# Performance work log

Hardware: AMD Instinct MI355X
Metric: run time of the kernel (lower is better)

## Reference

```python
import jax, jax.numpy as jnp
import numpy as np

B, T, D, H = 2, 4096, 768, 12
DK = D // H

def setup_inputs() -> dict:
    key = jax.random.key(0)
    ks = jax.random.split(key, 5)
    scale = 1.0 / np.sqrt(D)
    x = jax.random.normal(ks[0], (B, T, D), dtype=jnp.float32)
    WQ = jax.random.normal(ks[1], (D, D), dtype=jnp.float32) * scale
    WK = jax.random.normal(ks[2], (D, D), dtype=jnp.float32) * scale
    WV = jax.random.normal(ks[3], (D, D), dtype=jnp.float32) * scale
    Wproj = jax.random.normal(ks[4], (D, D), dtype=jnp.float32) * scale
    return {"x": x, "WQ": WQ, "WK": WK, "WV": WV, "Wproj": Wproj}

def reference(x, WQ, WK, WV, Wproj):
    # Weights stored as [in, out] (torch Linear weight transposed): y = x @ W
    def split_heads(y):
        return y.reshape(B, T, H, DK).transpose(0, 2, 1, 3)  # [B,H,T,DK]
    Q = split_heads(x @ WQ)
    K = split_heads(x @ WK)
    V = split_heads(x @ WV)
    score = jnp.einsum('bhqd,bhkd->bhqk', Q, K) * (DK ** -0.5)  # [B,H,T,T]
    attn = jax.nn.softmax(score, axis=-1)
    out = jnp.einsum('bhqk,bhkd->bhqd', attn, V)  # [B,H,T,DK]
    out = out.transpose(0, 2, 1, 3).reshape(B, T, D)
    return out @ Wproj
```

## Files before the change

### kernel.cpp

```cpp
#include <hip/hip_runtime.h>
#include <stdint.h>

#define B_ 2
#define T_ 4096
#define D_ 768
#define H_ 12
#define DK_ 64
#define BH_ 24

typedef unsigned short u16;
typedef unsigned int u32;
typedef __bf16 bf16x8 __attribute__((ext_vector_type(8)));
typedef float f32x4 __attribute__((ext_vector_type(4)));
typedef short s16x8 __attribute__((ext_vector_type(8)));

__device__ __forceinline__ float exp2_raw(float x) {
#if __has_builtin(__builtin_amdgcn_exp2f)
    return __builtin_amdgcn_exp2f(x);
#else
    float y; asm("v_exp_f32 %0, %1" : "=v"(y) : "v"(x)); return y;
#endif
}

__device__ __forceinline__ f32x4 mfma16(bf16x8 a, bf16x8 b, f32x4 c) {
    return __builtin_amdgcn_mfma_f32_16x16x32_bf16(a, b, c, 0, 0, 0);
}

__device__ __forceinline__ u16 f2bf(float f) {
    union { float f; u32 u; } v; v.f = f;
    u32 r = v.u + 0x7FFFu + ((v.u >> 16) & 1u);
    return (u16)(r >> 16);
}

__device__ __forceinline__ u32 pack2bf(float lo, float hi) {
    union { float f; u32 u; } a, b; a.f = lo; b.f = hi;
    return __builtin_amdgcn_perm(b.u + 0x8000u, a.u + 0x8000u, 0x07060302u);
}

__device__ __forceinline__ void gll16(const u16* g, u16* l) {
    __builtin_amdgcn_global_load_lds(
        (const __attribute__((address_space(1))) u32*)g,
        (__attribute__((address_space(3))) u32*)l, 16, 0, 0);
}

__global__ __launch_bounds__(256) void convert_x_kernel(
    const float* __restrict__ x, u16* __restrict__ xb)
{
    int i = (blockIdx.x * 256 + threadIdx.x) * 8;
    float4 a = *(const float4*)&x[i];
    float4 b = *(const float4*)&x[i + 4];
    uint4 dd;
    dd.x = pack2bf(a.x, a.y); dd.y = pack2bf(a.z, a.w);
    dd.z = pack2bf(b.x, b.y); dd.w = pack2bf(b.z, b.w);
    *(uint4*)&xb[i] = dd;
}

__global__ __launch_bounds__(256) void wtrans_kernel(
    const float* __restrict__ w0, const float* __restrict__ w1,
    const float* __restrict__ w2, const float* __restrict__ w3,
    u16* __restrict__ out)
{
    __shared__ u16 tile[32][33];
    const float* src = (blockIdx.z == 0) ? w0 : (blockIdx.z == 1) ? w1 : (blockIdx.z == 2) ? w2 : w3;
    u16* dst = out + (size_t)blockIdx.z * D_ * D_;
    int tx = threadIdx.x, ty = threadIdx.y;
    int x0 = blockIdx.x * 32, y0 = blockIdx.y * 32;
    for (int i = ty; i < 32; i += 8) tile[i][tx] = f2bf(src[(size_t)(y0 + i) * D_ + x0 + tx]);
    __syncthreads();
    for (int i = ty; i < 32; i += 8) dst[(size_t)(x0 + i) * D_ + y0 + tx] = tile[tx][i];
}

template<int MODE>
__global__ __launch_bounds__(256) void gemm_bt(
    const u16* __restrict__ A, const u16* __restrict__ Bt, void* __restrict__ outv)
{
    __shared__ u16 As[128 * 64];
    __shared__ u16 Bs[128 * 64];
    const int K = 768;
    int tid = threadIdx.x;
    int lane = tid & 63, wave = tid >> 6;
    int r = lane & 15, quad = lane >> 4;
    int rx = r & 7;
    int m0 = blockIdx.y * 128, n0 = blockIdx.x * 128;
    int wrow = (wave >> 1) * 64, wcol = (wave & 1) * 64;

    int srow = wave * 32 + (lane >> 3);
    int scol = ((lane & 7) ^ (lane >> 3)) * 8;
    const u16* Ag = A + (size_t)(m0 + srow) * K + scol;
    const u16* Bg = Bt + (size_t)(n0 + srow) * K + scol;

    f32x4 acc[4][4];
    #pragma unroll
    for (int i = 0; i < 4; i++)
        #pragma unroll
        for (int j = 0; j < 4; j++)
            #pragma unroll
            for (int e = 0; e < 4; e++) acc[i][j][e] = 0.f;

    for (int k0 = 0; k0 < K; k0 += 64) {
        __syncthreads();
        #pragma unroll
        for (int j = 0; j < 4; j++) {
            gll16(Ag + (size_t)j * 8 * K + k0, As + (wave * 32 + j * 8) * 64);
            gll16(Bg + (size_t)j * 8 * K + k0, Bs + (wave * 32 + j * 8) * 64);
        }
        __syncthreads();
        #pragma unroll
        for (int ks = 0; ks < 2; ks++) {
            int swz = ((ks * 4 + quad) ^ rx) * 8;
            bf16x8 af[4], bfr[4];
            #pragma unroll
            for (int mi = 0; mi < 4; mi++)
                af[mi] = *(const bf16x8*)&As[(wrow + mi * 16 + r) * 64 + swz];
            #pragma unroll
            for (int ni = 0; ni < 4; ni++)
                bfr[ni] = *(const bf16x8*)&Bs[(wcol + ni * 16 + r) * 64 + swz];
            #pragma unroll
            for (int mi = 0; mi < 4; mi++)
                #pragma unroll
                for (int ni = 0; ni < 4; ni++)
                    acc[mi][ni] = mfma16(af[mi], bfr[ni], acc[mi][ni]);
        }
    }

    if (MODE == 0) {
        u16* out = (u16*)outv;
        int which = n0 / D_;
        int nb = n0 % D_;
        const size_t HS = (size_t)B_ * H_ * T_ * DK_;
        if (which == 2) {
            u16* vt = out + 2 * HS;
            #pragma unroll
            for (int mi = 0; mi < 4; mi++) {
                int mg = m0 + wrow + mi * 16 + quad * 4;
                int b = mg >> 12, t = mg & 4095;
                #pragma unroll
                for (int ni = 0; ni < 4; ni++) {
                    int ng = nb + wcol + ni * 16 + r;
                    int h = ng >> 6, dk = ng & 63;
                    uint2 d;
                    d.x = pack2bf(acc[mi][ni][0], acc[mi][ni][1]);
                    d.y = pack2bf(acc[mi][ni][2], acc[mi][ni][3]);
                    *(uint2*)&vt[(((size_t)(b * H_ + h)) * DK_ + dk) * T_ + t] = d;
                }
            }
        } else {
            const float cf = (which == 0) ? 0.18033688011112042f : 1.0f;
            size_t wbase = (size_t)which * HS;
            #pragma unroll
            for (int mi = 0; mi < 4; mi++) {
                #pragma unroll
                for (int ni = 0; ni < 4; ni++) {
                    int ng = nb + wcol + ni * 16 + r;
                    int h = ng >> 6, dk = ng & 63;
                    #pragma unroll
                    for (int e = 0; e < 4; e++) {
                        int mg = m0 + wrow + mi * 16 + quad * 4 + e;
                        int b = mg >> 12, t = mg & 4095;
                        out[wbase + (((size_t)(b * H_ + h)) * T_ + t) * DK_ + dk]
                            = f2bf(acc[mi][ni][e] * cf);
                    }
                }
            }
        }
    } else {
        float* out = (float*)outv;
        #pragma unroll
        for (int mi = 0; mi < 4; mi++)
            #pragma unroll
            for (int ni = 0; ni < 4; ni++)
                #pragma unroll
                for (int e = 0; e < 4; e++)
                    out[(size_t)(m0 + wrow + mi * 16 + quad * 4 + e) * D_ + n0 + wcol + ni * 16 + r]
                        = acc[mi][ni][e];
    }
}

__global__ __launch_bounds__(256, 3) void attn_kernel(
    const u16* __restrict__ Q, const u16* __restrict__ K,
    const u16* __restrict__ VT, float* __restrict__ pO, float* __restrict__ pL)
{
    __shared__ u16 Ks[64 * 64];
    __shared__ u16 Vs[64 * 64];
    __shared__ u16 Pt[256 * 64];

    int tid = threadIdx.x;
    int lane = tid & 63, w = tid >> 6;
    int r = lane & 15, quad = lane >> 4;
    int rx = r & 7;
    int bh = blockIdx.y;
    int q0 = blockIdx.x * 256;
    int z = blockIdx.z;

    bf16x8 qf[4][2];
    #pragma unroll
    for (int qi = 0; qi < 4; qi++) {
        const u16* Qb = Q + ((size_t)bh * T_ + q0 + w * 64 + qi * 16 + r) * DK_;
        qf[qi][0] = *(const bf16x8*)(Qb + quad * 8);
        qf[qi][1] = *(const bf16x8*)(Qb + 32 + quad * 8);
    }

    bf16x8 ones;
    #pragma unroll
    for (int j = 0; j < 8; j++) ones[j] = (__bf16)1.0f;

    f32x4 o[4][4];
    f32x4 lacc[4];
    #pragma unroll
    for (int qi = 0; qi < 4; qi++) {
        #pragma unroll
        for (int e = 0; e < 4; e++) lacc[qi][e] = 0.f;
        #pragma unroll
        for (int n = 0; n < 4; n++)
            #pragma unroll
            for (int e = 0; e < 4; e++) o[qi][n][e] = 0.f;
    }

    u16* Pw = &Pt[w * 64 * 64];
    int kb0 = z * (T_ / 2), kb1 = kb0 + T_ / 2;

    for (int kb = kb0; kb < kb1; kb += 64) {
        __syncthreads();
        #pragma unroll
        for (int i = 0; i < 2; i++) {
            int c = tid + i * 256;
            int row = c >> 3, gc = c & 7;
            int lc = gc ^ (row & 7);
            *(bf16x8*)&Ks[row * 64 + lc * 8] =
                *(const bf16x8*)&K[((size_t)bh * T_ + kb + row) * DK_ + gc * 8];
            *(bf16x8*)&Vs[row * 64 + lc * 8] =
                *(const bf16x8*)&VT[((size_t)bh * DK_ + row) * T_ + kb + gc * 8];
        }
        __syncthreads();

        #pragma unroll
        for (int n = 0; n < 4; n++) {
            int krow = n * 16 + r;
            bf16x8 kf0 = *(const bf16x8*)&Ks[krow * 64 + ((quad ^ rx)) * 8];
            bf16x8 kf1 = *(const bf16x8*)&Ks[krow * 64 + (((4 + quad) ^ rx)) * 8];
            int c8 = 2 * n + (quad >> 1);
            #pragma unroll
            for (int qi = 0; qi < 4; qi++) {
                f32x4 zz;
                #pragma unroll
                for (int e = 0; e < 4; e++) zz[e] = 0.f;
                zz = mfma16(kf0, qf[qi][0], zz);
                zz = mfma16(kf1, qf[qi][1], zz);
                float p0 = exp2_raw(zz[0]), p1 = exp2_raw(zz[1]);
                float p2 = exp2_raw(zz[2]), p3 = exp2_raw(zz[3]);
                uint2 d;
                d.x = pack2bf(p0, p1);
                d.y = pack2bf(p2, p3);
                *(uint2*)&Pw[(qi * 16 + r) * 64 + (c8 ^ rx) * 8 + (quad & 1) * 4] = d;
            }
        }

        #pragma unroll
        for (int ks2 = 0; ks2 < 2; ks2++) {
            int swz = ((ks2 * 4 + quad) ^ rx) * 8;
            bf16x8 vf[4];
            #pragma unroll
            for (int ndk = 0; ndk < 4; ndk++)
                vf[ndk] = *(const bf16x8*)&Vs[(ndk * 16 + r) * 64 + swz];
            #pragma unroll
            for (int qi = 0; qi < 4; qi++) {
                bf16x8 pf = *(const bf16x8*)&Pw[(qi * 16 + r) * 64 + swz];
                lacc[qi] = mfma16(ones, pf, lacc[qi]);
                #pragma unroll
                for (int ndk = 0; ndk < 4; ndk++)
                    o[qi][ndk] = mfma16(vf[ndk], pf, o[qi][ndk]);
            }
        }
    }

    const size_t SP = (size_t)BH_ * T_ * DK_;
    #pragma unroll
    for (int qi = 0; qi < 4; qi++) {
        int q = q0 + w * 64 + qi * 16 + r;
        float* base = pO + (size_t)z * SP + ((size_t)bh * T_ + q) * DK_;
        #pragma unroll
        for (int ndk = 0; ndk < 4; ndk++)
            *(f32x4*)&base[ndk * 16 + quad * 4] = o[qi][ndk];
    }
    if (quad == 0) {
        #pragma unroll
        for (int qi = 0; qi < 4; qi++)
            pL[(size_t)z * BH_ * T_ + (size_t)bh * T_ + q0 + w * 64 + qi * 16 + r]
                = lacc[qi][0];
    }
}

__global__ __launch_bounds__(256) void combine_kernel(
    const float* __restrict__ pO, const float* __restrict__ pL, u16* __restrict__ AO)
{
    const size_t SP = (size_t)BH_ * T_ * DK_;
    int bh = blockIdx.y;
    int b = bh / H_, h = bh % H_;
    int q = blockIdx.x * 64 + (threadIdx.x >> 2);
    int dk0 = (threadIdx.x & 3) * 16;
    size_t idx = ((size_t)bh * T_ + q) * DK_ + dk0;
    float l0 = pL[(size_t)bh * T_ + q];
    float l1 = pL[(size_t)BH_ * T_ + (size_t)bh * T_ + q];
    float inv = 1.0f / (l0 + l1);
    u16* dst = AO + ((size_t)b * T_ + q) * D_ + h * DK_ + dk0;
    #pragma unroll
    for (int i = 0; i < 2; i++) {
        float4 a0 = *(const float4*)&pO[idx + i * 8];
        float4 a1 = *(const float4*)&pO[idx + i * 8 + 4];
        float4 b0 = *(const float4*)&pO[SP + idx + i * 8];
        float4 b1 = *(const float4*)&pO[SP + idx + i * 8 + 4];
        uint4 dd;
        dd.x = pack2bf((a0.x + b0.x) * inv, (a0.y + b0.y) * inv);
        dd.y = pack2bf((a0.z + b0.z) * inv, (a0.w + b0.w) * inv);
        dd.z = pack2bf((a1.x + b1.x) * inv, (a1.y + b1.y) * inv);
        dd.w = pack2bf((a1.z + b1.z) * inv, (a1.w + b1.w) * inv);
        *(uint4*)&dst[i * 8] = dd;
    }
}

extern "C" void kernel_launch(void* const* d_in, const int* in_sizes, int n_in,
                              void* d_out, int out_size, void* d_ws, size_t ws_size,
                              hipStream_t stream)
{
    const float* x  = (const float*)d_in[0];
    const float* wq = (const float*)d_in[1];
    const float* wk = (const float*)d_in[2];
    const float* wv = (const float*)d_in[3];
    const float* wp = (const float*)d_in[4];

    u16* ws = (u16*)d_ws;
    const size_t XS = (size_t)B_ * T_ * D_;
    const size_t WT = (size_t)D_ * D_;
    const size_t HS = (size_t)B_ * H_ * T_ * DK_;
    u16* xb = ws;
    u16* wt = xb + XS;
    u16* q  = wt + 4 * WT;
    u16* k  = q + HS;
    u16* vt = k + HS;
    u16* ao = vt + HS;
    float* pL = (float*)(ao + HS);
    float* pO = pL + 2 * (size_t)BH_ * T_;

    convert_x_kernel<<<dim3(3072), 256, 0, stream>>>(x, xb);
    wtrans_kernel<<<dim3(24, 24, 4), dim3(32, 8), 0, stream>>>(wq, wk, wv, wp, wt);
    gemm_bt<0><<<dim3(18, 64), 256, 0, stream>>>(xb, wt, q);
    attn_kernel<<<dim3(16, 24, 2), 256, 0, stream>>>(q, k, vt, pO, pL);
    combine_kernel<<<dim3(64, 24), 256, 0, stream>>>(pO, pL, ao);
    gemm_bt<1><<<dim3(6, 64), 256, 0, stream>>>(ao, wt + 3 * WT, d_out);
}
```

Before: 295.3 us.

## Split attention keys four ways, shrink P tile, store bf16 partials

The key range of the attention kernel is split four ways instead of two, doubling the number of blocks. The per-wave P staging buffer is halved by interleaving score computation and PV accumulation in two 32-key halves, and the occupancy hint rises from 3 to 5. K/V tiles are now loaded straight into LDS with global_load_lds instead of passing through registers. Partial outputs are written in bf16 and merged by a rewritten combine kernel, which cuts partial-sum traffic at the cost of some precision and extra combine reads.

Measured after the change: 1.122 ms. 3.8x slower.

```diff
diff --git a/kernel.cpp b/kernel.cpp
--- a/kernel.cpp
+++ b/kernel.cpp
@@ -7,6 +7,7 @@
 #define H_ 12
 #define DK_ 64
 #define BH_ 24
+#define ZSPLIT 4
 
 typedef unsigned short u16;
 typedef unsigned int u32;
@@ -30,6 +31,10 @@
     union { float f; u32 u; } v; v.f = f;
     u32 r = v.u + 0x7FFFu + ((v.u >> 16) & 1u);
     return (u16)(r >> 16);
+}
+
+__device__ __forceinline__ float bf2f(u16 u) {
+    union { u32 u; float f; } v; v.u = ((u32)u) << 16; return v.f;
 }
 
 __device__ __forceinline__ u32 pack2bf(float lo, float hi) {
@@ -176,18 +181,18 @@
     }
 }
 
-__global__ __launch_bounds__(256, 3) void attn_kernel(
+__global__ __launch_bounds__(256, 5) void attn_kernel(
     const u16* __restrict__ Q, const u16* __restrict__ K,
-    const u16* __restrict__ VT, float* __restrict__ pO, float* __restrict__ pL)
+    const u16* __restrict__ VT, u16* __restrict__ pOb, float* __restrict__ pL)
 {
     __shared__ u16 Ks[64 * 64];
     __shared__ u16 Vs[64 * 64];
-    __shared__ u16 Pt[256 * 64];
+    __shared__ u16 Pt[256 * 32];
 
     int tid = threadIdx.x;
     int lane = tid & 63, w = tid >> 6;
     int r = lane & 15, quad = lane >> 4;
-    int rx = r & 7;
+    int rx = r & 7, r3 = r & 3;
     int bh = blockIdx.y;
     int q0 = blockIdx.x * 256;
     int z = blockIdx.z;
@@ -216,55 +221,57 @@
             for (int e = 0; e < 4; e++) o[qi][n][e] = 0.f;
     }
 
-    u16* Pw = &Pt[w * 64 * 64];
-    int kb0 = z * (T_ / 2), kb1 = kb0 + T_ / 2;
-
-    for (int kb = kb0; kb < kb1; kb += 64) {
+    u16* Pw = &Pt[w * 64 * 32];
+
+    int sr = lane >> 3;
+    int gc = (lane & 7) ^ (sr & 7);
+    const u16* Kg = K + ((size_t)bh * T_ + w * 16 + sr) * DK_ + gc * 8;
+    const u16* Vg = VT + ((size_t)bh * DK_ + w * 16 + sr) * T_ + gc * 8;
+    u16* KsW = Ks + (w * 16) * 64;
+    u16* VsW = Vs + (w * 16) * 64;
+
+    int kb0 = z * (T_ / ZSPLIT);
+    for (int kb = kb0; kb < kb0 + T_ / ZSPLIT; kb += 64) {
         __syncthreads();
-        #pragma unroll
-        for (int i = 0; i < 2; i++) {
-            int c = tid + i * 256;
-            int row = c >> 3, gc = c & 7;
-            int lc = gc ^ (row & 7);
-            *(bf16x8*)&Ks[row * 64 + lc * 8] =
-                *(const bf16x8*)&K[((size_t)bh * T_ + kb + row) * DK_ + gc * 8];
-            *(bf16x8*)&Vs[row * 64 + lc * 8] =
-                *(const bf16x8*)&VT[((size_t)bh * DK_ + row) * T_ + kb + gc * 8];
-        }
+        gll16(Kg + (size_t)kb * DK_, KsW);
+        gll16(Kg + (size_t)kb * DK_ + 8 * DK_, KsW + 8 * 64);
+        gll16(Vg + kb, VsW);
+        gll16(Vg + kb + 8 * T_, VsW + 8 * 64);
         __syncthreads();
 
         #pragma unroll
-        for (int n = 0; n < 4; n++) {
-            int krow = n * 16 + r;
-            bf16x8 kf0 = *(const bf16x8*)&Ks[krow * 64 + ((quad ^ rx)) * 8];
-            bf16x8 kf1 = *(const bf16x8*)&Ks[krow * 64 + (((4 + quad) ^ rx)) * 8];
-            int c8 = 2 * n + (quad >> 1);
-            #pragma unroll
-            for (int qi = 0; qi < 4; qi++) {
-                f32x4 zz;
-                #pragma unroll
-                for (int e = 0; e < 4; e++) zz[e] = 0.f;
-                zz = mfma16(kf0, qf[qi][0], zz);
-                zz = mfma16(kf1, qf[qi][1], zz);
-                float p0 = exp2_raw(zz[0]), p1 = exp2_raw(zz[1]);
-                float p2 = exp2_raw(zz[2]), p3 = exp2_raw(zz[3]);
-                uint2 d;
-                d.x = pack2bf(p0, p1);
-                d.y = pack2bf(p2, p3);
-                *(uint2*)&Pw[(qi * 16 + r) * 64 + (c8 ^ rx) * 8 + (quad & 1) * 4] = d;
+        for (int half = 0; half < 2; half++) {
+            #pragma unroll
+            for (int n16 = 0; n16 < 2; n16++) {
+                int n = half * 2 + n16;
+                int krow = n * 16 + r;
+                bf16x8 kf0 = *(const bf16x8*)&Ks[krow * 64 + (quad ^ rx) * 8];
+                bf16x8 kf1 = *(const bf16x8*)&Ks[krow * 64 + ((4 + quad) ^ rx) * 8];
+                int slot = (n16 * 2 + (quad >> 1)) ^ r3;
+                #pragma unroll
+                for (int qi = 0; qi < 4; qi++) {
+                    f32x4 zz;
+                    #pragma unroll
+                    for (int e = 0; e < 4; e++) zz[e] = 0.f;
+                    zz = mfma16(kf0, qf[qi][0], zz);
+                    zz = mfma16(kf1, qf[qi][1], zz);
+                    float p0 = exp2_raw(zz[0]), p1 = exp2_raw(zz[1]);
+                    float p2 = exp2_raw(zz[2]), p3 = exp2_raw(zz[3]);
+                    uint2 d;
+                    d.x = pack2bf(p0, p1);
+                    d.y = pack2bf(p2, p3);
+                    *(uint2*)&Pw[(qi * 16 + r) * 32 + slot * 8 + (quad & 1) * 4] = d;
+                }
             }
-        }
-
-        #pragma unroll
-        for (int ks2 = 0; ks2 < 2; ks2++) {
-            int swz = ((ks2 * 4 + quad) ^ rx) * 8;
+            int swz = ((half * 4 + quad) ^ rx) * 8;
             bf16x8 vf[4];
             #pragma unroll
             for (int ndk = 0; ndk < 4; ndk++)
                 vf[ndk] = *(const bf16x8*)&Vs[(ndk * 16 + r) * 64 + swz];
+            int pslot = (quad ^ r3) * 8;
             #pragma unroll
             for (int qi = 0; qi < 4; qi++) {
-                bf16x8 pf = *(const bf16x8*)&Pw[(qi * 16 + r) * 64 + swz];
+                bf16x8 pf = *(const bf16x8*)&Pw[(qi * 16 + r) * 32 + pslot];
                 lacc[qi] = mfma16(ones, pf, lacc[qi]);
                 #pragma unroll
                 for (int ndk = 0; ndk < 4; ndk++)
@@ -277,10 +284,14 @@
     #pragma unroll
     for (int qi = 0; qi < 4; qi++) {
         int q = q0 + w * 64 + qi * 16 + r;
-        float* base = pO + (size_t)z * SP + ((size_t)bh * T_ + q) * DK_;
-        #pragma unroll
-        for (int ndk = 0; ndk < 4; ndk++)
-            *(f32x4*)&base[ndk * 16 + quad * 4] = o[qi][ndk];
+        u16* base = pOb + (size_t)z * SP + ((size_t)bh * T_ + q) * DK_;
+        #pragma unroll
+        for (int ndk = 0; ndk < 4; ndk++) {
+            uint2 d;
+            d.x = pack2bf(o[qi][ndk][0], o[qi][ndk][1]);
+            d.y = pack2bf(o[qi][ndk][2], o[qi][ndk][3]);
+            *(uint2*)&base[ndk * 16 + quad * 4] = d;
+        }
     }
     if (quad == 0) {
         #pragma unroll
@@ -291,31 +302,35 @@
 }
 
 __global__ __launch_bounds__(256) void combine_kernel(
-    const float* __restrict__ pO, const float* __restrict__ pL, u16* __restrict__ AO)
+    const u16* __restrict__ pOb, const float* __restrict__ pL, u16* __restrict__ AO)
 {
     const size_t SP = (size_t)BH_ * T_ * DK_;
     int bh = blockIdx.y;
     int b = bh / H_, h = bh % H_;
-    int q = blockIdx.x * 64 + (threadIdx.x >> 2);
-    int dk0 = (threadIdx.x & 3) * 16;
+    int f = blockIdx.x * 256 + threadIdx.x;
+    int q = f >> 3, dk0 = (f & 7) * 8;
     size_t idx = ((size_t)bh * T_ + q) * DK_ + dk0;
-    float l0 = pL[(size_t)bh * T_ + q];
-    float l1 = pL[(size_t)BH_ * T_ + (size_t)bh * T_ + q];
-    float inv = 1.0f / (l0 + l1);
-    u16* dst = AO + ((size_t)b * T_ + q) * D_ + h * DK_ + dk0;
-    #pragma unroll
-    for (int i = 0; i < 2; i++) {
-        float4 a0 = *(const float4*)&pO[idx + i * 8];
-        float4 a1 = *(const float4*)&pO[idx + i * 8 + 4];
-        float4 b0 = *(const float4*)&pO[SP + idx + i * 8];
-        float4 b1 = *(const float4*)&pO[SP + idx + i * 8 + 4];
-        uint4 dd;
-        dd.x = pack2bf((a0.x + b0.x) * inv, (a0.y + b0.y) * inv);
-        dd.y = pack2bf((a0.z + b0.z) * inv, (a0.w + b0.w) * inv);
-        dd.z = pack2bf((a1.x + b1.x) * inv, (a1.y + b1.y) * inv);
-        dd.w = pack2bf((a1.z + b1.z) * inv, (a1.w + b1.w) * inv);
-        *(uint4*)&dst[i * 8] = dd;
-    }
+
+    float l = 0.f;
+    #pragma unroll
+    for (int z = 0; z < ZSPLIT; z++) l += pL[(size_t)z * BH_ * T_ + (size_t)bh * T_ + q];
+    float inv = 1.0f / l;
+
+    float acc[8];
+    #pragma unroll
+    for (int e = 0; e < 8; e++) acc[e] = 0.f;
+    #pragma unroll
+    for (int z = 0; z < ZSPLIT; z++) {
+        s16x8 v = *(const s16x8*)&pOb[(size_t)z * SP + idx];
+        #pragma unroll
+        for (int e = 0; e < 8; e++) acc[e] += bf2f((u16)v[e]);
+    }
+    uint4 dd;
+    dd.x = pack2bf(acc[0] * inv, acc[1] * inv);
+    dd.y = pack2bf(acc[2] * inv, acc[3] * inv);
+    dd.z = pack2bf(acc[4] * inv, acc[5] * inv);
+    dd.w = pack2bf(acc[6] * inv, acc[7] * inv);
+    *(uint4*)&AO[((size_t)b * T_ + q) * D_ + h * DK_ + dk0] = dd;
 }
 
 extern "C" void kernel_launch(void* const* d_in, const int* in_sizes, int n_in,
@@ -339,12 +354,12 @@
     u16* vt = k + HS;
     u16* ao = vt + HS;
     float* pL = (float*)(ao + HS);
-    float* pO = pL + 2 * (size_t)BH_ * T_;
+    u16* pOb = (u16*)(pL + (size_t)ZSPLIT * BH_ * T_);
 
     convert_x_kernel<<<dim3(3072), 256, 0, stream>>>(x, xb);
     wtrans_kernel<<<dim3(24, 24, 4), dim3(32, 8), 0, stream>>>(wq, wk, wv, wp, wt);
     gemm_bt<0><<<dim3(18, 64), 256, 0, stream>>>(xb, wt, q);
-    attn_kernel<<<dim3(16, 24, 2), 256, 0, stream>>>(q, k, vt, pO, pL);
-    combine_kernel<<<dim3(64, 24), 256, 0, stream>>>(pO, pL, ao);
-    gemm_bt<1><<<dim3(6, 64), 256, 0, stream>>>(ao, wt + 3 * WT, d_out);
-}
+    attn_kernel<<<dim3(16, 24, ZSPLIT), 256, 0, stream>>>(q, k, vt, pOb, pL);
+    combine_kernel<<<dim3(128, 24), 256, 0, stream>>>(pOb, pL, ao);
+    gemm_bt<1><<<dim3(6, 64), 256, 0, stream>>>(ao, wt + 3 * WT, (u16*)d_out);
+}
```
